# Performance work log

Hardware: AMD Instinct MI355X
Metric: run time of the kernel (lower is better)

The kernel has to match this reference:

```python
import jax, jax.numpy as jnp
import numpy as np

N, C, EMB_ROWS = 524288, 128, 32
SLOPE = 0.2  # leaky_relu negative slope


def setup_inputs() -> dict:
    key = jax.random.key(0)
    k1, k2, k3, k4, k5 = jax.random.split(key, 5)
    x = jax.random.normal(k1, (N, C), jnp.float32)
    perm = jax.random.permutation(k2, N)  # fixed stand-in for torch.randperm
    depth = jax.random.normal(k3, (EMB_ROWS, 128), jnp.float32)  # Embedding(32,128), N(0,1) init
    fan_in = 2 * C * 2
    bound = 1.0 / np.sqrt(fan_in)
    W = jax.random.uniform(k4, (C, 2 * C, 2), jnp.float32, -bound, bound)  # Conv1d weight (O,I,K)
    b = jax.random.uniform(k5, (C,), jnp.float32, -bound, bound)
    return {"x": x, "depth": depth, "W": W, "b": b, "perm": perm}


def reference(x, depth, W, b, perm):
    c = W.shape[0]
    x = x[perm]                      # random shuffle of rows
    x = x.T.reshape(1, c, -1)        # [1, C, N]
    i = 0
    # Python while over STATIC shapes -> unrolled at trace time (~log2(N) steps)
    while x.shape[-1] > 1:
        L = x.shape[-1]
        e = jnp.broadcast_to(depth[i].reshape(1, 128, 1), (1, 128, L))
        x = jnp.concatenate([x, e], axis=1)   # [1, 2C, L]
        x = jax.lax.conv_general_dilated(
            x, W, window_strides=(1,), padding="VALID",
            dimension_numbers=("NCH", "OIH", "NCH"))  # [1, C, L-1]
        x = x + b.reshape(1, -1, 1)
        x = jnp.where(x >= 0, x, SLOPE * x)   # leaky_relu(0.2)
        if x.shape[-1] == 1:
            break
        # MaxPool1d(2,2): floor(L/2), drops trailing element for odd L
        x = jax.lax.reduce_window(
            x, -jnp.inf, jax.lax.max,
            window_dimensions=(1, 1, 2), window_strides=(1, 1, 2),
            padding="VALID")
        i += 1
    return x.reshape(c, 1).T  # [1, C]
```

## Files before the change

### kernel.cpp

```cpp
#include <hip/hip_runtime.h>
#include <hip/hip_bf16.h>


typedef __bf16 v8bf __attribute__((ext_vector_type(8)));
typedef float v16f __attribute__((ext_vector_type(16)));

__device__ __forceinline__ ushort f2bf(float f) {
    __hip_bfloat16 h = __float2bfloat16(f);
    return *reinterpret_cast<ushort*>(&h);
}
__device__ __forceinline__ unsigned pack2(float lo, float hi) {
    return (unsigned)f2bf(lo) | ((unsigned)f2bf(hi) << 16);
}
__device__ __forceinline__ float leaky(float y) { return (y >= 0.f) ? y : 0.2f * y; }

#define ZACC {0.f,0.f,0.f,0.f,0.f,0.f,0.f,0.f,0.f,0.f,0.f,0.f,0.f,0.f,0.f,0.f}

__global__ void bias_kernel(const float* __restrict__ W, const float* __restrict__ b,
                            const float* __restrict__ depth, float* __restrict__ Bst) {
    int i = blockIdx.x, o = threadIdx.x;
    const float* Wo = W + (size_t)o * 512 + 256;
    const float* di = depth + (size_t)i * 128;
    float s = b[o];
#pragma unroll 8
    for (int c = 0; c < 128; ++c) s += di[c] * (Wo[2 * c] + Wo[2 * c + 1]);
    Bst[i * 128 + o] = s;
}

__global__ void repack_kernel(const float* __restrict__ W, ushort* __restrict__ A) {
    int o = blockIdx.x, c = threadIdx.x;
    float v = (c < 128) ? W[(size_t)o * 512 + 2 * c] : W[(size_t)o * 512 + 2 * (c - 128) + 1];
    A[o * 256 + c] = f2bf(v);
}

#define WAVE_SETUP()                                                          \
    const int tid = threadIdx.x;                                              \
    const int lane = tid & 63;                                                \
    const int w = tid >> 6;                                                   \
    const int n31 = lane & 31;                                                \
    const int h = lane >> 5;                                                  \
    v8bf af[16];                                                              \
    {                                                                         \
        const ushort* Arow = A + (size_t)(w * 32 + n31) * 256 + h * 8;        \
        _Pragma("unroll")                                                     \
        for (int s = 0; s < 16; ++s) af[s] = *(const v8bf*)&Arow[s * 16];     \
    }

#define LOAD_BIAS(dst_, Bs)                                                   \
    float dst_[16];                                                           \
    _Pragma("unroll")                                                         \
    for (int r = 0; r < 16; ++r)                                              \
        dst_[r] = (Bs)[w * 32 + (r & 3) + 8 * (r >> 2) + 4 * h];

#define MFMA_TILE_LDS(buf, r0_, r1_, acc)                                     \
    {                                                                         \
        const ushort* sp0 = (buf) + (r0_) * 128;                              \
        const ushort* sp1 = (buf) + (r1_) * 128;                              \
        const int mm0 = (r0_) & 15, mm1 = (r1_) & 15;                         \
        _Pragma("unroll")                                                     \
        for (int s = 0; s < 8; ++s)                                           \
            acc = __builtin_amdgcn_mfma_f32_32x32x16_bf16(                    \
                af[s], *(const v8bf*)&sp0[((2 * s + h) ^ mm0) * 8], acc, 0, 0, 0); \
        _Pragma("unroll")                                                     \
        for (int s = 0; s < 8; ++s)                                           \
            acc = __builtin_amdgcn_mfma_f32_32x32x16_bf16(                    \
                af[8 + s], *(const v8bf*)&sp1[((2 * s + h) ^ mm1) * 8], acc, 0, 0, 0); \
    }

__global__ __launch_bounds__(256)
void pair_fused(const ushort* __restrict__ Xin,
                const float* __restrict__ x0,
                const int* __restrict__ perm,
                const ushort* __restrict__ A,
                const float* __restrict__ Bst2,
                ushort* __restrict__ Y,
                int Lin, int Lp2, int stage0) {
    __shared__ __align__(16) ushort xin[132 * 128];
    __shared__ __align__(16) ushort mid[65 * 128];
    __shared__ int prow[132];

    const int U = blockIdx.x * 32;
    const int t0 = U * 4;

    if (stage0) {
        for (int r = threadIdx.x; r < 132; r += 256)
            prow[r] = perm[min(t0 + r, Lin - 1)];
        __syncthreads();
    }
    for (int idx = threadIdx.x; idx < 132 * 16; idx += 256) {
        int row = idx >> 4, ck = idx & 15;
        int t = min(t0 + row, Lin - 1);
        int dst = row * 128 + ((ck ^ (row & 15)) * 8);
        if (stage0) {
            const float* s = x0 + (size_t)prow[row] * 128 + ck * 8;
            float4 a = *(const float4*)s;
            float4 bq = *(const float4*)(s + 4);
            uint4 v;
            v.x = pack2(a.x, a.y);  v.y = pack2(a.z, a.w);
            v.z = pack2(bq.x, bq.y); v.w = pack2(bq.z, bq.w);
            *(uint4*)&xin[dst] = v;
        } else {
            *(uint4*)&xin[dst] = *(const uint4*)&Xin[(size_t)t * 128 + ck * 8];
        }
    }
    __syncthreads();

    WAVE_SETUP();

    {
        LOAD_BIAS(bias_r, Bst2);
#pragma unroll
        for (int ti = 0; ti < 5; ++ti) {
            const int p = 32 * ti + n31;
            const int r0 = min(p, 131), r1 = min(p + 1, 131);
            v16f acc = ZACC;
            MFMA_TILE_LDS(xin, r0, r1, acc);
            const int u1 = 16 * ti + (n31 >> 1);
            const bool act = !(lane & 1) && (u1 < 65);
#pragma unroll
            for (int q = 0; q < 4; ++q) {
                float pv[4];
#pragma unroll
                for (int j = 0; j < 4; ++j) {
                    float y = leaky(acc[4 * q + j] + bias_r[4 * q + j]);
                    float y2 = __shfl_xor(y, 1, 64);
                    pv[j] = fmaxf(y, y2);
                }
                if (act) {
                    uint2 v;
                    v.x = pack2(pv[0], pv[1]);
                    v.y = pack2(pv[2], pv[3]);
                    *(uint2*)&mid[u1 * 128 + (((4 * w + q) ^ (u1 & 15)) * 8) + 4 * h] = v;
                }
            }
        }
    }
    __syncthreads();

    {
        LOAD_BIAS(bias_r, Bst2 + 128);
#pragma unroll
        for (int ti = 0; ti < 2; ++ti) {
            const int p = 32 * ti + n31;
            v16f acc = ZACC;
            MFMA_TILE_LDS(mid, p, p + 1, acc);
            const int u2 = U + 16 * ti + (n31 >> 1);
            const bool act = !(lane & 1) && (u2 < Lp2);
#pragma unroll
            for (int q = 0; q < 4; ++q) {
                float pv[4];
#pragma unroll
                for (int j = 0; j < 4; ++j) {
                    float y = leaky(acc[4 * q + j] + bias_r[4 * q + j]);
                    float y2 = __shfl_xor(y, 1, 64);
                    pv[j] = fmaxf(y, y2);
                }
                if (act) {
                    uint2 v;
                    v.x = pack2(pv[0], pv[1]);
                    v.y = pack2(pv[2], pv[3]);
                    *(uint2*)&Y[(size_t)u2 * 128 + w * 32 + 8 * q + 4 * h] = v;
                }
            }
        }
    }
}

__global__ __launch_bounds__(1024)
void tail_fused(const ushort* __restrict__ Xg, const ushort* __restrict__ A,
                const float* __restrict__ BstAll, float* __restrict__ out) {
    extern __shared__ __align__(16) ushort tbuf[];
    ushort* buf0 = tbuf;
    ushort* buf1 = tbuf + 255 * 128;

    const int tid = threadIdx.x;
    const int lane = tid & 63;
    const int wv = tid >> 6;
    const int w = wv & 3;
    const int wp = wv >> 2;
    const int n31 = lane & 31;
    const int h = lane >> 5;
    v8bf af[16];
    {
        const ushort* Arow = A + (size_t)(w * 32 + n31) * 256 + h * 8;
#pragma unroll
        for (int s = 0; s < 16; ++s) af[s] = *(const v8bf*)&Arow[s * 16];
    }

    int Lin = 511;
    for (int st = 0; st < 8; ++st) {
        const int Lp = (Lin - 1) >> 1;
        LOAD_BIAS(bias_r, BstAll + (size_t)(10 + st) * 128);
        ushort* dst = (st & 1) ? buf1 : buf0;
        const ushort* src = (st & 1) ? buf0 : buf1;
        const int ntiles = (Lin - 1 + 31) >> 5;
        for (int ti = wp; ti < ntiles; ti += 4) {
            const int t = ti * 32 + n31;
            const int r0 = min(t, Lin - 1), r1 = min(t + 1, Lin - 1);
            v16f acc = ZACC;
            if (st == 0) {
                const ushort* p0 = Xg + (size_t)r0 * 128 + h * 8;
                const ushort* p1 = Xg + (size_t)r1 * 128 + h * 8;
#pragma unroll
                for (int s = 0; s < 8; ++s)
                    acc = __builtin_amdgcn_mfma_f32_32x32x16_bf16(
                        af[s], *(const v8bf*)&p0[s * 16], acc, 0, 0, 0);
#pragma unroll
                for (int s = 0; s < 8; ++s)
                    acc = __builtin_amdgcn_mfma_f32_32x32x16_bf16(
                        af[8 + s], *(const v8bf*)&p1[s * 16], acc, 0, 0, 0);
            } else {
                MFMA_TILE_LDS(src, r0, r1, acc);
            }
            const int u = t >> 1;
            const bool act = !(lane & 1) && (u < Lp);
#pragma unroll
            for (int q = 0; q < 4; ++q) {
                float pv[4];
#pragma unroll
                for (int j = 0; j < 4; ++j) {
                    float y = leaky(acc[4 * q + j] + bias_r[4 * q + j]);
                    float y2 = __shfl_xor(y, 1, 64);
                    pv[j] = fmaxf(y, y2);
                }
                if (act) {
                    if (st < 7) {
                        uint2 v;
                        v.x = pack2(pv[0], pv[1]);
                        v.y = pack2(pv[2], pv[3]);
                        *(uint2*)&dst[u * 128 + (((4 * w + q) ^ (u & 15)) * 8) + 4 * h] = v;
                    } else {
                        float4 o = {pv[0], pv[1], pv[2], pv[3]};
                        *(float4*)&out[w * 32 + 8 * q + 4 * h] = o;
                    }
                }
            }
        }
        __syncthreads();
        Lin = Lp;
    }
}

extern "C" void kernel_launch(void* const* d_in, const int* in_sizes, int n_in,
                              void* d_out, int out_size, void* d_ws, size_t ws_size,
                              hipStream_t stream) {
    const float* x     = (const float*)d_in[0];
    const float* depth = (const float*)d_in[1];
    const float* W     = (const float*)d_in[2];
    const float* b     = (const float*)d_in[3];
    const int*   perm  = (const int*)d_in[4];
    float* out = (float*)d_out;

    char* ws = (char*)d_ws;
    float*  Bst = (float*)ws;
    ushort* A   = (ushort*)(ws + 16384);
    ushort* R0  = (ushort*)(ws + 16384 + 65536);
    ushort* R1  = (ushort*)(ws + 16384 + 65536 + (size_t)131071 * 256);

    bias_kernel<<<18, 128, 0, stream>>>(W, b, depth, Bst);
    repack_kernel<<<128, 256, 0, stream>>>(W, A);

    pair_fused<<<4096, 256, 0, stream>>>(nullptr, x, perm, A, Bst, R0,
                                         524288, 131071, 1);
    pair_fused<<<1024, 256, 0, stream>>>(R0, nullptr, nullptr, A, Bst + 2 * 128, R1,
                                         131071, 32767, 0);
    pair_fused<<<256, 256, 0, stream>>>(R1, nullptr, nullptr, A, Bst + 4 * 128, R0,
                                        32767, 8191, 0);
    pair_fused<<<64, 256, 0, stream>>>(R0, nullptr, nullptr, A, Bst + 6 * 128, R1,
                                       8191, 2047, 0);
    pair_fused<<<16, 256, 0, stream>>>(R1, nullptr, nullptr, A, Bst + 8 * 128, R0,
                                       2047, 511, 0);
    tail_fused<<<1, 1024, (255 + 127) * 128 * 2, stream>>>(R0, A, Bst, out);
}
```

Measured before the change: 543.5 us.

## Fuse three conv-pool stages per kernel and merge prep kernels

```diff
diff --git a/kernel.cpp b/kernel.cpp
--- a/kernel.cpp
+++ b/kernel.cpp
@@ -16,21 +16,26 @@
 
 #define ZACC {0.f,0.f,0.f,0.f,0.f,0.f,0.f,0.f,0.f,0.f,0.f,0.f,0.f,0.f,0.f,0.f}
 
-__global__ void bias_kernel(const float* __restrict__ W, const float* __restrict__ b,
-                            const float* __restrict__ depth, float* __restrict__ Bst) {
-    int i = blockIdx.x, o = threadIdx.x;
-    const float* Wo = W + (size_t)o * 512 + 256;
-    const float* di = depth + (size_t)i * 128;
-    float s = b[o];
+__global__ __launch_bounds__(256)
+void prep_kernel(const float* __restrict__ W, const float* __restrict__ b,
+                 const float* __restrict__ depth, float* __restrict__ Bst,
+                 ushort* __restrict__ A) {
+    if (blockIdx.x < 18) {
+        if (threadIdx.x < 128) {
+            int i = blockIdx.x, o = threadIdx.x;
+            const float* Wo = W + (size_t)o * 512 + 256;
+            const float* di = depth + (size_t)i * 128;
+            float s = b[o];
 #pragma unroll 8
-    for (int c = 0; c < 128; ++c) s += di[c] * (Wo[2 * c] + Wo[2 * c + 1]);
-    Bst[i * 128 + o] = s;
-}
-
-__global__ void repack_kernel(const float* __restrict__ W, ushort* __restrict__ A) {
-    int o = blockIdx.x, c = threadIdx.x;
-    float v = (c < 128) ? W[(size_t)o * 512 + 2 * c] : W[(size_t)o * 512 + 2 * (c - 128) + 1];
-    A[o * 256 + c] = f2bf(v);
+            for (int c = 0; c < 128; ++c) s += di[c] * (Wo[2 * c] + Wo[2 * c + 1]);
+            Bst[i * 128 + o] = s;
+        }
+    } else {
+        int o = blockIdx.x - 18, c = threadIdx.x;
+        float v = (c < 128) ? W[(size_t)o * 512 + 2 * c]
+                            : W[(size_t)o * 512 + 2 * (c - 128) + 1];
+        A[o * 256 + c] = f2bf(v);
+    }
 }
 
 #define WAVE_SETUP()                                                          \
@@ -65,6 +70,24 @@
         for (int s = 0; s < 8; ++s)                                           \
             acc = __builtin_amdgcn_mfma_f32_32x32x16_bf16(                    \
                 af[8 + s], *(const v8bf*)&sp1[((2 * s + h) ^ mm1) * 8], acc, 0, 0, 0); \
+    }
+
+#define POOL_STORE_LDS(dstbuf, u_, guard_)                                    \
+    _Pragma("unroll")                                                         \
+    for (int q = 0; q < 4; ++q) {                                             \
+        float pv[4];                                                          \
+        _Pragma("unroll")                                                     \
+        for (int j = 0; j < 4; ++j) {                                         \
+            float y = leaky(acc[4 * q + j] + bias_r[4 * q + j]);              \
+            float y2 = __shfl_xor(y, 1, 64);                                  \
+            pv[j] = fmaxf(y, y2);                                             \
+        }                                                                     \
+        if (guard_) {                                                         \
+            uint2 v;                                                          \
+            v.x = pack2(pv[0], pv[1]);                                        \
+            v.y = pack2(pv[2], pv[3]);                                        \
+            *(uint2*)&(dstbuf)[(u_) * 128 + (((4 * w + q) ^ ((u_) & 15)) * 8) + 4 * h] = v; \
+        }                                                                     \
     }
 
 __global__ __launch_bounds__(256)
@@ -117,22 +140,7 @@
             MFMA_TILE_LDS(xin, r0, r1, acc);
             const int u1 = 16 * ti + (n31 >> 1);
             const bool act = !(lane & 1) && (u1 < 65);
-#pragma unroll
-            for (int q = 0; q < 4; ++q) {
-                float pv[4];
-#pragma unroll
-                for (int j = 0; j < 4; ++j) {
-                    float y = leaky(acc[4 * q + j] + bias_r[4 * q + j]);
-                    float y2 = __shfl_xor(y, 1, 64);
-                    pv[j] = fmaxf(y, y2);
-                }
-                if (act) {
-                    uint2 v;
-                    v.x = pack2(pv[0], pv[1]);
-                    v.y = pack2(pv[2], pv[3]);
-                    *(uint2*)&mid[u1 * 128 + (((4 * w + q) ^ (u1 & 15)) * 8) + 4 * h] = v;
-                }
-            }
+            POOL_STORE_LDS(mid, u1, act);
         }
     }
     __syncthreads();
@@ -160,6 +168,88 @@
                     v.x = pack2(pv[0], pv[1]);
                     v.y = pack2(pv[2], pv[3]);
                     *(uint2*)&Y[(size_t)u2 * 128 + w * 32 + 8 * q + 4 * h] = v;
+                }
+            }
+        }
+    }
+}
+
+__global__ __launch_bounds__(256)
+void tri_fused(const ushort* __restrict__ Xin,
+               const ushort* __restrict__ A,
+               const float* __restrict__ Bst3,
+               ushort* __restrict__ Y,
+               int Lin, int Lp3) {
+    __shared__ __align__(16) ushort bin[264 * 128];
+    __shared__ __align__(16) ushort m1[131 * 128];
+
+    const int U = blockIdx.x * 32;
+    const int t0 = U * 8;
+
+    for (int idx = threadIdx.x; idx < 264 * 16; idx += 256) {
+        int row = idx >> 4, ck = idx & 15;
+        int t = min(t0 + row, Lin - 1);
+        *(uint4*)&bin[row * 128 + ((ck ^ (row & 15)) * 8)] =
+            *(const uint4*)&Xin[(size_t)t * 128 + ck * 8];
+    }
+    __syncthreads();
+
+    WAVE_SETUP();
+
+    {
+        LOAD_BIAS(bias_r, Bst3);
+#pragma unroll
+        for (int ti = 0; ti < 9; ++ti) {
+            const int p = 32 * ti + n31;
+            const int r0 = min(p, 263), r1 = min(p + 1, 263);
+            v16f acc = ZACC;
+            MFMA_TILE_LDS(bin, r0, r1, acc);
+            const int u1 = 16 * ti + (n31 >> 1);
+            const bool act = !(lane & 1) && (u1 < 131);
+            POOL_STORE_LDS(m1, u1, act);
+        }
+    }
+    __syncthreads();
+
+    ushort* m2 = bin;
+    {
+        LOAD_BIAS(bias_r, Bst3 + 128);
+#pragma unroll
+        for (int ti = 0; ti < 5; ++ti) {
+            const int p = 32 * ti + n31;
+            const int r0 = min(p, 130), r1 = min(p + 1, 130);
+            v16f acc = ZACC;
+            MFMA_TILE_LDS(m1, r0, r1, acc);
+            const int u2 = 16 * ti + (n31 >> 1);
+            const bool act = !(lane & 1) && (u2 < 65);
+            POOL_STORE_LDS(m2, u2, act);
+        }
+    }
+    __syncthreads();
+
+    {
+        LOAD_BIAS(bias_r, Bst3 + 256);
+#pragma unroll
+        for (int ti = 0; ti < 2; ++ti) {
+            const int p = 32 * ti + n31;
+            v16f acc = ZACC;
+            MFMA_TILE_LDS(m2, p, p + 1, acc);
+            const int u3 = U + 16 * ti + (n31 >> 1);
+            const bool act = !(lane & 1) && (u3 < Lp3);
+#pragma unroll
+            for (int q = 0; q < 4; ++q) {
+                float pv[4];
+#pragma unroll
+                for (int j = 0; j < 4; ++j) {
+                    float y = leaky(acc[4 * q + j] + bias_r[4 * q + j]);
+                    float y2 = __shfl_xor(y, 1, 64);
+                    pv[j] = fmaxf(y, y2);
+                }
+                if (act) {
+                    uint2 v;
+                    v.x = pack2(pv[0], pv[1]);
+                    v.y = pack2(pv[2], pv[3]);
+                    *(uint2*)&Y[(size_t)u3 * 128 + w * 32 + 8 * q + 4 * h] = v;
                 }
             }
         }
@@ -257,18 +347,13 @@
     ushort* R0  = (ushort*)(ws + 16384 + 65536);
     ushort* R1  = (ushort*)(ws + 16384 + 65536 + (size_t)131071 * 256);
 
-    bias_kernel<<<18, 128, 0, stream>>>(W, b, depth, Bst);
-    repack_kernel<<<128, 256, 0, stream>>>(W, A);
+    prep_kernel<<<146, 256, 0, stream>>>(W, b, depth, Bst, A);
 
     pair_fused<<<4096, 256, 0, stream>>>(nullptr, x, perm, A, Bst, R0,
                                          524288, 131071, 1);
-    pair_fused<<<1024, 256, 0, stream>>>(R0, nullptr, nullptr, A, Bst + 2 * 128, R1,
-                                         131071, 32767, 0);
-    pair_fused<<<256, 256, 0, stream>>>(R1, nullptr, nullptr, A, Bst + 4 * 128, R0,
-                                        32767, 8191, 0);
-    pair_fused<<<64, 256, 0, stream>>>(R0, nullptr, nullptr, A, Bst + 6 * 128, R1,
-                                       8191, 2047, 0);
-    pair_fused<<<16, 256, 0, stream>>>(R1, nullptr, nullptr, A, Bst + 8 * 128, R0,
+    tri_fused<<<512, 256, 0, stream>>>(R0, A, Bst + 2 * 128, R1, 131071, 16383);
+    tri_fused<<<64, 256, 0, stream>>>(R1, A, Bst + 5 * 128, R0, 16383, 2047);
+    pair_fused<<<16, 256, 0, stream>>>(R0, nullptr, nullptr, A, Bst + 8 * 128, R1,
                                        2047, 511, 0);
-    tail_fused<<<1, 1024, (255 + 127) * 128 * 2, stream>>>(R0, A, Bst, out);
-}
+    tail_fused<<<1, 1024, (255 + 127) * 128 * 2, stream>>>(R1, A, Bst, out);
+}
```

After: 552.5 us. About the same (+1.7%).
